# Optimization experiments

Measured on AMD Instinct MI355X. Metric: run time of the kernel, lower is better.

Reference implementation:

```python
import jax, jax.numpy as jnp
import numpy as np

C = 256
CQK = C // 8  # 32


def setup_inputs() -> dict:
    key = jax.random.key(0)
    ks = jax.random.split(key, 7)
    x = jax.random.normal(ks[0], (4, C, 64, 64), dtype=jnp.float32)
    s = 1.0 / np.sqrt(C)
    Wq = jax.random.normal(ks[1], (CQK, C), dtype=jnp.float32) * s
    bq = jnp.zeros((CQK,), dtype=jnp.float32)
    Wk = jax.random.normal(ks[2], (CQK, C), dtype=jnp.float32) * s
    bk = jnp.zeros((CQK,), dtype=jnp.float32)
    Wv = jax.random.normal(ks[3], (C, C), dtype=jnp.float32) * s
    bv = jnp.zeros((C,), dtype=jnp.float32)
    return {"x": x, "Wq": Wq, "bq": bq, "Wk": Wk, "bk": bk, "Wv": Wv, "bv": bv}


def reference(x, Wq, bq, Wk, bk, Wv, bv):
    B, Cc, H, W = x.shape
    xf = x.reshape(B, Cc, H * W)  # [B, C, HW]
    # 1x1 convs == per-pixel linear projections over channels
    q = jnp.einsum('oc,bcn->bno', Wq, xf) + bq          # [B, HW, C//8]
    k = jnp.einsum('oc,bcn->bon', Wk, xf) + bk[:, None]  # [B, C//8, HW]
    v = jnp.einsum('oc,bcn->bno', Wv, xf) + bv          # [B, HW, C]
    attn = jax.nn.softmax(jnp.einsum('bnd,bdm->bnm', q, k), axis=-1)  # [B, HW, HW]
    out = jnp.einsum('bnm,bmc->bnc', attn, v)           # [B, HW, C]
    return out.transpose(0, 2, 1).reshape(B, Cc, H, W)
```

## Files before the change

kernel.cpp:

```cpp
#include <hip/hip_runtime.h>
#include <hip/hip_bf16.h>


#define N_PIX 4096
#define DQK   32
#define CCH   256
#define LOG2E 1.44269504088896f

typedef __attribute__((ext_vector_type(8))) _Float16 f16x8;
typedef __attribute__((ext_vector_type(4))) _Float16 f16x4;
typedef __attribute__((ext_vector_type(2))) _Float16 f16x2;
typedef __attribute__((ext_vector_type(8))) short    bf16x8;
typedef __attribute__((ext_vector_type(4))) short    bf16x4;
typedef __attribute__((ext_vector_type(4))) float    f32x4;

__device__ inline void barrier_lds() {
    asm volatile("" ::: "memory");
    __builtin_amdgcn_s_waitcnt(0xc07f);
    __builtin_amdgcn_s_barrier();
    asm volatile("" ::: "memory");
}

__device__ inline short bf16bits(float f) {
    __hip_bfloat16 h = __float2bfloat16(f);
    return *(short*)&h;
}

__global__ __launch_bounds__(256) void wpack_kernel(
    const float* __restrict__ Wq, const float* __restrict__ Wk,
    const float* __restrict__ Wv, _Float16* __restrict__ Wp)
{
    const int tid   = threadIdx.x;
    const int wflat = blockIdx.x * 4 + (tid >> 6);
    const int lane  = tid & 63;
    const int L15   = lane & 15;
    const int quad  = lane >> 4;
    const int mt    = wflat >> 3;
    const int ks    = wflat & 7;
    const int m0    = mt * 16;

    const float* Wsrc; int row; float scale = 1.f;
    if (m0 < 32)      { Wsrc = Wq; row = m0 + L15;      scale = LOG2E; }
    else if (m0 < 64) { Wsrc = Wk; row = m0 - 32 + L15; }
    else              { Wsrc = Wv; row = m0 - 64 + L15; }

    const float* p = Wsrc + (size_t)row * 256 + ks * 32 + quad * 8;
    f16x8 h;
    #pragma unroll
    for (int j = 0; j < 8; ++j) h[j] = (_Float16)(p[j] * scale);
    *(f16x8*)(Wp + ((size_t)wflat * 64 + lane) * 8) = h;
}

__global__ __launch_bounds__(512, 4) void qkv_kernel(
    const float* __restrict__ x, const _Float16* __restrict__ Wp,
    const float* __restrict__ bq, const float* __restrict__ bk,
    const float* __restrict__ bv,
    _Float16* __restrict__ qo, _Float16* __restrict__ ko,
    __hip_bfloat16* __restrict__ vp)
{
    __shared__ alignas(16) unsigned char shraw[256 * 40 * 2];
    _Float16       (*xT)[264] = (_Float16 (*)[264])shraw;
    __hip_bfloat16 (*vst)[40] = (__hip_bfloat16 (*)[40])shraw;

    const int idx = blockIdx.x;
    const int b   = (idx & 7) >> 1;
    const int n0  = (((idx >> 3) << 1) | (idx & 1)) * 32;
    const int tid = threadIdx.x;

    {
        const float* xb = x + (size_t)b * CCH * N_PIX;
        float4 ld[2][2];
        int c2s[2], n4s[2];
        #pragma unroll
        for (int pass = 0; pass < 2; ++pass) {
            const int flat = pass * 512 + tid;
            c2s[pass] = (flat >> 3) * 2;
            n4s[pass] = (flat & 7) * 4;
            ld[pass][0] = *(const float4*)(xb + (size_t)c2s[pass]       * N_PIX + n0 + n4s[pass]);
            ld[pass][1] = *(const float4*)(xb + (size_t)(c2s[pass] + 1) * N_PIX + n0 + n4s[pass]);
        }
        #pragma unroll
        for (int pass = 0; pass < 2; ++pass) {
            const float a[4] = {ld[pass][0].x, ld[pass][0].y, ld[pass][0].z, ld[pass][0].w};
            const float c[4] = {ld[pass][1].x, ld[pass][1].y, ld[pass][1].z, ld[pass][1].w};
            #pragma unroll
            for (int i = 0; i < 4; ++i)
                *(f16x2*)(&xT[n4s[pass] + i][c2s[pass]]) =
                    (f16x2){(_Float16)a[i], (_Float16)c[i]};
        }
    }
    __syncthreads();

    const int lane = tid & 63;
    const int wid  = tid >> 6;
    const int L15  = lane & 15;
    const int quad = lane >> 4;
    const int nf   = wid & 1;
    const int mtg  = wid >> 1;

    const f32x4 fz = {0.f, 0.f, 0.f, 0.f};
    f32x4 acc[5];
    #pragma unroll
    for (int mt = 0; mt < 5; ++mt) acc[mt] = fz;

    const _Float16* wpw = Wp + ((size_t)(mtg * 5) * 8 * 64 + lane) * 8;

    #pragma unroll
    for (int ks = 0; ks < 8; ++ks) {
        const f16x8 bfr = *(const f16x8*)(&xT[nf * 16 + L15][ks * 32 + quad * 8]);
        #pragma unroll
        for (int mt = 0; mt < 5; ++mt) {
            const f16x8 afr = *(const f16x8*)(wpw + (size_t)(mt * 8 + ks) * 512);
            acc[mt] = __builtin_amdgcn_mfma_f32_16x16x32_f16(afr, bfr, acc[mt], 0, 0, 0);
        }
    }

    const int np = nf * 16 + L15;
    const int n  = n0 + np;
    #pragma unroll
    for (int mt = 0; mt < 5; ++mt) {
        const int m0 = (mtg * 5 + mt) * 16;
        const f32x4 a = acc[mt];
        if (m0 < 32) {
            const int mr = m0 + quad * 4;
            f16x4 h;
            #pragma unroll
            for (int r = 0; r < 4; ++r) h[r] = (_Float16)(a[r] + bq[mr + r] * LOG2E);
            *(f16x4*)(qo + ((size_t)b * N_PIX + n) * DQK + mr) = h;
        } else if (m0 < 64) {
            const int mr = m0 - 32 + quad * 4;
            f16x4 h;
            #pragma unroll
            for (int r = 0; r < 4; ++r) h[r] = (_Float16)(a[r] + bk[mr + r]);
            *(f16x4*)(ko + ((size_t)b * N_PIX + n) * DQK + mr) = h;
        }
    }

    __syncthreads();

    #pragma unroll
    for (int mt = 0; mt < 5; ++mt) {
        const int m0 = (mtg * 5 + mt) * 16;
        if (m0 >= 64) {
            const int c = m0 - 64 + quad * 4;
            #pragma unroll
            for (int r = 0; r < 4; ++r)
                vst[c + r][np] = __float2bfloat16(acc[mt][r] + bv[c + r]);
        }
    }
    __syncthreads();

    {
        __hip_bfloat16* vpb = vp + (size_t)b * 2048 * 512 + (size_t)((n0 >> 5) * 16) * 512;
        #pragma unroll
        for (int s = 0; s < 2; ++s) {
            const int slot = s * 512 + tid;
            const int cg16 = slot >> 6;
            const int ln   = slot & 63;
            const int qd   = ln >> 4;
            const int l15  = ln & 15;
            const bf16x8 val = *(const bf16x8*)(&vst[cg16 * 16 + l15][qd * 8]);
            *(bf16x8*)(vpb + ((size_t)cg16 * 64 + ln) * 8) = val;
        }
    }
}

__global__ __launch_bounds__(1024, 1) void attn_kernel(
    const _Float16* __restrict__ qg,
    const _Float16* __restrict__ kg,
    const __hip_bfloat16* __restrict__ vp,
    float* __restrict__ out)
{
    __shared__ alignas(16) __hip_bfloat16 Ps[2][64][72];
    __shared__ float lsum[4][4][16];

    const int idx  = blockIdx.x;
    const int b    = (idx & 7) >> 1;
    const int n0   = (((idx >> 3) << 1) | (idx & 1)) * 64;
    const int tid  = threadIdx.x;
    const int wid  = tid >> 6;
    const int lane = tid & 63;
    const int L15  = lane & 15;
    const int quad = lane >> 4;
    const int qt   = wid & 3;
    const int kt   = wid >> 2;
    const int qp   = wid & 1;
    const int cg   = wid >> 1;
    const int c0   = cg * 32;

    const f32x4 fz = {0.f, 0.f, 0.f, 0.f};

    const f16x8 aq = *(const f16x8*)(qg + ((size_t)b * N_PIX + n0 + qt * 16 + L15) * DQK + quad * 8);

    f32x4 oacc[2][2];
    #pragma unroll
    for (int qq = 0; qq < 2; ++qq)
        #pragma unroll
        for (int cf = 0; cf < 2; ++cf) oacc[qq][cf] = fz;
    float psum = 0.f;

    const _Float16* kptr =
        kg + (size_t)b * N_PIX * DQK + (size_t)(kt * 16 + L15) * DQK + quad * 8;
    const __hip_bfloat16* vpb = vp + (size_t)b * 2048 * 512 + (size_t)lane * 8;

    const f16x8 k0f = *(const f16x8*)kptr;
    f16x8 kcur = *(const f16x8*)(kptr + 64 * DQK);
    bf16x8 vcur[2][2], vnext[2][2];
    #pragma unroll
    for (int kk = 0; kk < 2; ++kk)
        #pragma unroll
        for (int cf = 0; cf < 2; ++cf) {
            vcur[kk][cf]  = *(const bf16x8*)(vpb + (size_t)((kk)*16     + cg * 2 + cf) * 512);
            vnext[kk][cf] = *(const bf16x8*)(vpb + (size_t)((2 + kk)*16 + cg * 2 + cf) * 512);
        }
    {
        const f32x4 s = __builtin_amdgcn_mfma_f32_16x16x32_f16(k0f, aq, fz, 0, 0, 0);
        bf16x4 pk;
        #pragma unroll
        for (int r = 0; r < 4; ++r) { const float p = exp2f(s[r]); psum += p; pk[r] = bf16bits(p); }
        *(bf16x4*)(&Ps[0][qt * 16 + L15][kt * 16 + quad * 4]) = pk;
    }
    barrier_lds();

    for (int it = 0; it < 64; ++it) {
        const int buf = it & 1;
        const int ld  = (it + 2 < 64) ? it + 2 : 63;

        const f16x8 knew = *(const f16x8*)(kptr + (size_t)ld * 64 * DQK);
        bf16x8 vnew[2][2];
        #pragma unroll
        for (int kk = 0; kk < 2; ++kk)
            #pragma unroll
            for (int cf = 0; cf < 2; ++cf)
                vnew[kk][cf] = *(const bf16x8*)(vpb + (size_t)((ld * 2 + kk) * 16 + cg * 2 + cf) * 512);

        #pragma unroll
        for (int qq = 0; qq < 2; ++qq)
            #pragma unroll
            for (int kk = 0; kk < 2; ++kk) {
                const bf16x8 ap = *(const bf16x8*)(&Ps[buf][(qp * 2 + qq) * 16 + L15][kk * 32 + quad * 8]);
                #pragma unroll
                for (int cf = 0; cf < 2; ++cf)
                    oacc[qq][cf] = __builtin_amdgcn_mfma_f32_16x16x32_bf16(ap, vcur[kk][cf], oacc[qq][cf], 0, 0, 0);
            }

        if (it < 63) {
            const f32x4 s = __builtin_amdgcn_mfma_f32_16x16x32_f16(kcur, aq, fz, 0, 0, 0);
            bf16x4 pk;
            #pragma unroll
            for (int r = 0; r < 4; ++r) { const float p = exp2f(s[r]); psum += p; pk[r] = bf16bits(p); }
            *(bf16x4*)(&Ps[buf ^ 1][qt * 16 + L15][kt * 16 + quad * 4]) = pk;
        }
        barrier_lds();

        kcur = knew;
        #pragma unroll
        for (int kk = 0; kk < 2; ++kk)
            #pragma unroll
            for (int cf = 0; cf < 2; ++cf) {
                vcur[kk][cf]  = vnext[kk][cf];
                vnext[kk][cf] = vnew[kk][cf];
            }
    }

    psum += __shfl_xor(psum, 16, 64);
    psum += __shfl_xor(psum, 32, 64);
    if (quad == 0) lsum[qt][kt][L15] = psum;
    __syncthreads();

    float* ob = out + (size_t)b * CCH * N_PIX;
    #pragma unroll
    for (int qq = 0; qq < 2; ++qq) {
        const int qtile = qp * 2 + qq;
        float inv_l[4];
        #pragma unroll
        for (int r = 0; r < 4; ++r) {
            const int q = quad * 4 + r;
            inv_l[r] = 1.f / (lsum[qtile][0][q] + lsum[qtile][1][q] +
                              lsum[qtile][2][q] + lsum[qtile][3][q]);
        }
        #pragma unroll
        for (int cf = 0; cf < 2; ++cf) {
            const int c = c0 + cf * 16 + L15;
            f32x4 o;
            #pragma unroll
            for (int r = 0; r < 4; ++r) o[r] = oacc[qq][cf][r] * inv_l[r];
            *(f32x4*)(ob + (size_t)c * N_PIX + n0 + qtile * 16 + quad * 4) = o;
        }
    }
}

extern "C" void kernel_launch(void* const* d_in, const int* in_sizes, int n_in,
                              void* d_out, int out_size, void* d_ws, size_t ws_size,
                              hipStream_t stream) {
    (void)in_sizes; (void)n_in; (void)out_size; (void)ws_size;
    const float* x  = (const float*)d_in[0];
    const float* Wq = (const float*)d_in[1];
    const float* bq = (const float*)d_in[2];
    const float* Wk = (const float*)d_in[3];
    const float* bk = (const float*)d_in[4];
    const float* Wv = (const float*)d_in[5];
    const float* bv = (const float*)d_in[6];

    _Float16* qb = (_Float16*)d_ws;
    _Float16* kb = qb + (size_t)4 * N_PIX * DQK;
    __hip_bfloat16* vpk = (__hip_bfloat16*)(kb + (size_t)4 * N_PIX * DQK);
    _Float16* wp = (_Float16*)(vpk + (size_t)4 * 2048 * 512);
    float* outp = (float*)d_out;

    wpack_kernel<<<40, 256, 0, stream>>>(Wq, Wk, Wv, wp);
    qkv_kernel<<<512, 512, 0, stream>>>(x, wp, bq, bk, bv, qb, kb, vpk);
    attn_kernel<<<256, 1024, 0, stream>>>(qb, kb, vpk, outp);
}
```

Baseline: 147.4 us.

## Fuse weight pack, QKV projection and attention into one cooperative kernel

Merges the three launches (weight packing, QKV projection, attention) into a single cooperative kernel of 256 blocks of 1024 threads, separated by grid-wide syncs. Each block now projects 64 pixels instead of 32 and reuses one shared-memory buffer for all phases. The goal is to remove launch gaps and inter-kernel drain and fill. In exchange it adds two grid barriers, and the QKV phase gets fewer, larger blocks with lower occupancy. It also adds an unroll-2 pragma on the attention loop.

```diff
diff --git a/kernel.cpp b/kernel.cpp
--- a/kernel.cpp
+++ b/kernel.cpp
@@ -1,5 +1,8 @@
 #include <hip/hip_runtime.h>
 #include <hip/hip_bf16.h>
+#include <hip/hip_cooperative_groups.h>
+
+namespace cg = cooperative_groups;
 
 
 #define N_PIX 4096
@@ -26,266 +29,251 @@
     return *(short*)&h;
 }
 
-__global__ __launch_bounds__(256) void wpack_kernel(
-    const float* __restrict__ Wq, const float* __restrict__ Wk,
-    const float* __restrict__ Wv, _Float16* __restrict__ Wp)
-{
-    const int tid   = threadIdx.x;
-    const int wflat = blockIdx.x * 4 + (tid >> 6);
-    const int lane  = tid & 63;
-    const int L15   = lane & 15;
-    const int quad  = lane >> 4;
-    const int mt    = wflat >> 3;
-    const int ks    = wflat & 7;
-    const int m0    = mt * 16;
-
-    const float* Wsrc; int row; float scale = 1.f;
-    if (m0 < 32)      { Wsrc = Wq; row = m0 + L15;      scale = LOG2E; }
-    else if (m0 < 64) { Wsrc = Wk; row = m0 - 32 + L15; }
-    else              { Wsrc = Wv; row = m0 - 64 + L15; }
-
-    const float* p = Wsrc + (size_t)row * 256 + ks * 32 + quad * 8;
-    f16x8 h;
-    #pragma unroll
-    for (int j = 0; j < 8; ++j) h[j] = (_Float16)(p[j] * scale);
-    *(f16x8*)(Wp + ((size_t)wflat * 64 + lane) * 8) = h;
-}
-
-__global__ __launch_bounds__(512, 4) void qkv_kernel(
-    const float* __restrict__ x, const _Float16* __restrict__ Wp,
-    const float* __restrict__ bq, const float* __restrict__ bk,
-    const float* __restrict__ bv,
+__global__ __launch_bounds__(1024, 1) void fused_kernel(
+    const float* __restrict__ x,
+    const float* __restrict__ Wq, const float* __restrict__ bq,
+    const float* __restrict__ Wk, const float* __restrict__ bk,
+    const float* __restrict__ Wv, const float* __restrict__ bv,
     _Float16* __restrict__ qo, _Float16* __restrict__ ko,
-    __hip_bfloat16* __restrict__ vp)
-{
-    __shared__ alignas(16) unsigned char shraw[256 * 40 * 2];
-    _Float16       (*xT)[264] = (_Float16 (*)[264])shraw;
-    __hip_bfloat16 (*vst)[40] = (__hip_bfloat16 (*)[40])shraw;
-
-    const int idx = blockIdx.x;
-    const int b   = (idx & 7) >> 1;
-    const int n0  = (((idx >> 3) << 1) | (idx & 1)) * 32;
-    const int tid = threadIdx.x;
-
-    {
-        const float* xb = x + (size_t)b * CCH * N_PIX;
-        float4 ld[2][2];
-        int c2s[2], n4s[2];
-        #pragma unroll
-        for (int pass = 0; pass < 2; ++pass) {
-            const int flat = pass * 512 + tid;
-            c2s[pass] = (flat >> 3) * 2;
-            n4s[pass] = (flat & 7) * 4;
-            ld[pass][0] = *(const float4*)(xb + (size_t)c2s[pass]       * N_PIX + n0 + n4s[pass]);
-            ld[pass][1] = *(const float4*)(xb + (size_t)(c2s[pass] + 1) * N_PIX + n0 + n4s[pass]);
-        }
-        #pragma unroll
-        for (int pass = 0; pass < 2; ++pass) {
-            const float a[4] = {ld[pass][0].x, ld[pass][0].y, ld[pass][0].z, ld[pass][0].w};
-            const float c[4] = {ld[pass][1].x, ld[pass][1].y, ld[pass][1].z, ld[pass][1].w};
-            #pragma unroll
-            for (int i = 0; i < 4; ++i)
-                *(f16x2*)(&xT[n4s[pass] + i][c2s[pass]]) =
-                    (f16x2){(_Float16)a[i], (_Float16)c[i]};
-        }
-    }
-    __syncthreads();
-
-    const int lane = tid & 63;
-    const int wid  = tid >> 6;
-    const int L15  = lane & 15;
-    const int quad = lane >> 4;
-    const int nf   = wid & 1;
-    const int mtg  = wid >> 1;
-
-    const f32x4 fz = {0.f, 0.f, 0.f, 0.f};
-    f32x4 acc[5];
-    #pragma unroll
-    for (int mt = 0; mt < 5; ++mt) acc[mt] = fz;
-
-    const _Float16* wpw = Wp + ((size_t)(mtg * 5) * 8 * 64 + lane) * 8;
-
-    #pragma unroll
-    for (int ks = 0; ks < 8; ++ks) {
-        const f16x8 bfr = *(const f16x8*)(&xT[nf * 16 + L15][ks * 32 + quad * 8]);
-        #pragma unroll
-        for (int mt = 0; mt < 5; ++mt) {
-            const f16x8 afr = *(const f16x8*)(wpw + (size_t)(mt * 8 + ks) * 512);
-            acc[mt] = __builtin_amdgcn_mfma_f32_16x16x32_f16(afr, bfr, acc[mt], 0, 0, 0);
-        }
-    }
-
-    const int np = nf * 16 + L15;
-    const int n  = n0 + np;
-    #pragma unroll
-    for (int mt = 0; mt < 5; ++mt) {
-        const int m0 = (mtg * 5 + mt) * 16;
-        const f32x4 a = acc[mt];
-        if (m0 < 32) {
-            const int mr = m0 + quad * 4;
-            f16x4 h;
-            #pragma unroll
-            for (int r = 0; r < 4; ++r) h[r] = (_Float16)(a[r] + bq[mr + r] * LOG2E);
-            *(f16x4*)(qo + ((size_t)b * N_PIX + n) * DQK + mr) = h;
-        } else if (m0 < 64) {
-            const int mr = m0 - 32 + quad * 4;
-            f16x4 h;
-            #pragma unroll
-            for (int r = 0; r < 4; ++r) h[r] = (_Float16)(a[r] + bk[mr + r]);
-            *(f16x4*)(ko + ((size_t)b * N_PIX + n) * DQK + mr) = h;
-        }
-    }
-
-    __syncthreads();
-
-    #pragma unroll
-    for (int mt = 0; mt < 5; ++mt) {
-        const int m0 = (mtg * 5 + mt) * 16;
-        if (m0 >= 64) {
-            const int c = m0 - 64 + quad * 4;
-            #pragma unroll
-            for (int r = 0; r < 4; ++r)
-                vst[c + r][np] = __float2bfloat16(acc[mt][r] + bv[c + r]);
-        }
-    }
-    __syncthreads();
-
-    {
-        __hip_bfloat16* vpb = vp + (size_t)b * 2048 * 512 + (size_t)((n0 >> 5) * 16) * 512;
-        #pragma unroll
-        for (int s = 0; s < 2; ++s) {
-            const int slot = s * 512 + tid;
-            const int cg16 = slot >> 6;
-            const int ln   = slot & 63;
-            const int qd   = ln >> 4;
-            const int l15  = ln & 15;
-            const bf16x8 val = *(const bf16x8*)(&vst[cg16 * 16 + l15][qd * 8]);
-            *(bf16x8*)(vpb + ((size_t)cg16 * 64 + ln) * 8) = val;
-        }
-    }
-}
-
-__global__ __launch_bounds__(1024, 1) void attn_kernel(
-    const _Float16* __restrict__ qg,
-    const _Float16* __restrict__ kg,
-    const __hip_bfloat16* __restrict__ vp,
+    __hip_bfloat16* __restrict__ vp,
+    _Float16* __restrict__ Wp,
     float* __restrict__ out)
 {
-    __shared__ alignas(16) __hip_bfloat16 Ps[2][64][72];
-    __shared__ float lsum[4][4][16];
+    __shared__ alignas(16) unsigned char shraw[36864];
+    _Float16       (*xT)[264]     = (_Float16 (*)[264])shraw;
+    __hip_bfloat16 (*vst)[72]     = (__hip_bfloat16 (*)[72])shraw;
+    __hip_bfloat16 (*Ps)[64][72]  = (__hip_bfloat16 (*)[64][72])shraw;
+    float          (*lsum)[4][16] = (float (*)[4][16])(shraw + 2 * 64 * 72 * 2);
 
     const int idx  = blockIdx.x;
-    const int b    = (idx & 7) >> 1;
-    const int n0   = (((idx >> 3) << 1) | (idx & 1)) * 64;
     const int tid  = threadIdx.x;
     const int wid  = tid >> 6;
     const int lane = tid & 63;
     const int L15  = lane & 15;
     const int quad = lane >> 4;
-    const int qt   = wid & 3;
-    const int kt   = wid >> 2;
-    const int qp   = wid & 1;
-    const int cg   = wid >> 1;
-    const int c0   = cg * 32;
+
+    const int b  = (idx & 7) >> 1;
+    const int nt = ((idx >> 3) << 1) | (idx & 1);
+    const int n0 = nt * 64;
 
     const f32x4 fz = {0.f, 0.f, 0.f, 0.f};
 
-    const f16x8 aq = *(const f16x8*)(qg + ((size_t)b * N_PIX + n0 + qt * 16 + L15) * DQK + quad * 8);
-
-    f32x4 oacc[2][2];
-    #pragma unroll
-    for (int qq = 0; qq < 2; ++qq)
-        #pragma unroll
-        for (int cf = 0; cf < 2; ++cf) oacc[qq][cf] = fz;
-    float psum = 0.f;
-
-    const _Float16* kptr =
-        kg + (size_t)b * N_PIX * DQK + (size_t)(kt * 16 + L15) * DQK + quad * 8;
-    const __hip_bfloat16* vpb = vp + (size_t)b * 2048 * 512 + (size_t)lane * 8;
-
-    const f16x8 k0f = *(const f16x8*)kptr;
-    f16x8 kcur = *(const f16x8*)(kptr + 64 * DQK);
-    bf16x8 vcur[2][2], vnext[2][2];
-    #pragma unroll
-    for (int kk = 0; kk < 2; ++kk)
-        #pragma unroll
-        for (int cf = 0; cf < 2; ++cf) {
-            vcur[kk][cf]  = *(const bf16x8*)(vpb + (size_t)((kk)*16     + cg * 2 + cf) * 512);
-            vnext[kk][cf] = *(const bf16x8*)(vpb + (size_t)((2 + kk)*16 + cg * 2 + cf) * 512);
-        }
     {
-        const f32x4 s = __builtin_amdgcn_mfma_f32_16x16x32_f16(k0f, aq, fz, 0, 0, 0);
-        bf16x4 pk;
-        #pragma unroll
-        for (int r = 0; r < 4; ++r) { const float p = exp2f(s[r]); psum += p; pk[r] = bf16bits(p); }
-        *(bf16x4*)(&Ps[0][qt * 16 + L15][kt * 16 + quad * 4]) = pk;
+        const float* xb = x + (size_t)b * CCH * N_PIX;
+        float4 ld[2][2];
+        int c2s[2], n4s[2];
+        #pragma unroll
+        for (int pass = 0; pass < 2; ++pass) {
+            const int flat = pass * 1024 + tid;
+            c2s[pass] = (flat >> 4) * 2;
+            n4s[pass] = (flat & 15) * 4;
+            ld[pass][0] = *(const float4*)(xb + (size_t)c2s[pass]       * N_PIX + n0 + n4s[pass]);
+            ld[pass][1] = *(const float4*)(xb + (size_t)(c2s[pass] + 1) * N_PIX + n0 + n4s[pass]);
+        }
+        #pragma unroll
+        for (int pass = 0; pass < 2; ++pass) {
+            const float a[4] = {ld[pass][0].x, ld[pass][0].y, ld[pass][0].z, ld[pass][0].w};
+            const float c[4] = {ld[pass][1].x, ld[pass][1].y, ld[pass][1].z, ld[pass][1].w};
+            #pragma unroll
+            for (int i = 0; i < 4; ++i)
+                *(f16x2*)(&xT[n4s[pass] + i][c2s[pass]]) =
+                    (f16x2){(_Float16)a[i], (_Float16)c[i]};
+        }
     }
-    barrier_lds();
-
-    for (int it = 0; it < 64; ++it) {
-        const int buf = it & 1;
-        const int ld  = (it + 2 < 64) ? it + 2 : 63;
-
-        const f16x8 knew = *(const f16x8*)(kptr + (size_t)ld * 64 * DQK);
-        bf16x8 vnew[2][2];
+
+    if (idx < 10) {
+        const int wflat = idx * 16 + wid;
+        const int mt    = wflat >> 3;
+        const int ks    = wflat & 7;
+        const int m0    = mt * 16;
+        const float* Wsrc; int row; float scale = 1.f;
+        if (m0 < 32)      { Wsrc = Wq; row = m0 + L15;      scale = LOG2E; }
+        else if (m0 < 64) { Wsrc = Wk; row = m0 - 32 + L15; }
+        else              { Wsrc = Wv; row = m0 - 64 + L15; }
+        const float* p = Wsrc + (size_t)row * 256 + ks * 32 + quad * 8;
+        f16x8 h;
+        #pragma unroll
+        for (int j = 0; j < 8; ++j) h[j] = (_Float16)(p[j] * scale);
+        *(f16x8*)(Wp + ((size_t)wflat * 64 + lane) * 8) = h;
+    }
+
+    cg::this_grid().sync();
+
+    {
+        const int nf  = wid & 3;
+        const int mtg = wid >> 2;
+
+        f32x4 acc[5];
+        #pragma unroll
+        for (int mt = 0; mt < 5; ++mt) acc[mt] = fz;
+
+        const _Float16* wpw = Wp + ((size_t)(mtg * 5) * 8 * 64 + lane) * 8;
+
+        #pragma unroll
+        for (int ks = 0; ks < 8; ++ks) {
+            const f16x8 bfr = *(const f16x8*)(&xT[nf * 16 + L15][ks * 32 + quad * 8]);
+            #pragma unroll
+            for (int mt = 0; mt < 5; ++mt) {
+                const f16x8 afr = *(const f16x8*)(wpw + (size_t)(mt * 8 + ks) * 512);
+                acc[mt] = __builtin_amdgcn_mfma_f32_16x16x32_f16(afr, bfr, acc[mt], 0, 0, 0);
+            }
+        }
+
+        const int np = nf * 16 + L15;
+        const int n  = n0 + np;
+        #pragma unroll
+        for (int mt = 0; mt < 5; ++mt) {
+            const int m0 = (mtg * 5 + mt) * 16;
+            const f32x4 a = acc[mt];
+            if (m0 < 32) {
+                const int mr = m0 + quad * 4;
+                f16x4 h;
+                #pragma unroll
+                for (int r = 0; r < 4; ++r) h[r] = (_Float16)(a[r] + bq[mr + r] * LOG2E);
+                *(f16x4*)(qo + ((size_t)b * N_PIX + n) * DQK + mr) = h;
+            } else if (m0 < 64) {
+                const int mr = m0 - 32 + quad * 4;
+                f16x4 h;
+                #pragma unroll
+                for (int r = 0; r < 4; ++r) h[r] = (_Float16)(a[r] + bk[mr + r]);
+                *(f16x4*)(ko + ((size_t)b * N_PIX + n) * DQK + mr) = h;
+            }
+        }
+
+        __syncthreads();
+
+        #pragma unroll
+        for (int mt = 0; mt < 5; ++mt) {
+            const int m0 = (mtg * 5 + mt) * 16;
+            if (m0 >= 64) {
+                const int c = m0 - 64 + quad * 4;
+                #pragma unroll
+                for (int r = 0; r < 4; ++r)
+                    vst[c + r][np] = __float2bfloat16(acc[mt][r] + bv[c + r]);
+            }
+        }
+        __syncthreads();
+
+        __hip_bfloat16* vpb0 = vp + (size_t)b * 2048 * 512 + (size_t)(nt * 2) * 16 * 512;
+        #pragma unroll
+        for (int s = 0; s < 2; ++s) {
+            const int slot = s * 1024 + tid;
+            const int nch  = slot >> 10;
+            const int rem  = slot & 1023;
+            const int cg16 = rem >> 6;
+            const int ln   = rem & 63;
+            const bf16x8 val = *(const bf16x8*)(&vst[cg16 * 16 + (ln & 15)][nch * 32 + (ln >> 4) * 8]);
+            *(bf16x8*)(vpb0 + ((size_t)(nch * 16 + cg16) * 64 + ln) * 8) = val;
+        }
+    }
+
+    cg::this_grid().sync();
+
+    {
+        const int qt = wid & 3;
+        const int kt = wid >> 2;
+        const int qp = wid & 1;
+        const int cg = wid >> 1;
+        const int c0 = cg * 32;
+
+        const f16x8 aq = *(const f16x8*)(qo + ((size_t)b * N_PIX + n0 + qt * 16 + L15) * DQK + quad * 8);
+
+        f32x4 oacc[2][2];
+        #pragma unroll
+        for (int qq = 0; qq < 2; ++qq)
+            #pragma unroll
+            for (int cf = 0; cf < 2; ++cf) oacc[qq][cf] = fz;
+        float psum = 0.f;
+
+        const _Float16* kptr =
+            ko + (size_t)b * N_PIX * DQK + (size_t)(kt * 16 + L15) * DQK + quad * 8;
+        const __hip_bfloat16* vpb = vp + (size_t)b * 2048 * 512 + (size_t)lane * 8;
+
+        const f16x8 k0f = *(const f16x8*)kptr;
+        f16x8 kcur = *(const f16x8*)(kptr + 64 * DQK);
+        bf16x8 vcur[2][2], vnext[2][2];
         #pragma unroll
         for (int kk = 0; kk < 2; ++kk)
             #pragma unroll
-            for (int cf = 0; cf < 2; ++cf)
-                vnew[kk][cf] = *(const bf16x8*)(vpb + (size_t)((ld * 2 + kk) * 16 + cg * 2 + cf) * 512);
-
-        #pragma unroll
-        for (int qq = 0; qq < 2; ++qq)
-            #pragma unroll
-            for (int kk = 0; kk < 2; ++kk) {
-                const bf16x8 ap = *(const bf16x8*)(&Ps[buf][(qp * 2 + qq) * 16 + L15][kk * 32 + quad * 8]);
+            for (int cf = 0; cf < 2; ++cf) {
+                vcur[kk][cf]  = *(const bf16x8*)(vpb + (size_t)(kk * 16       + cg * 2 + cf) * 512);
+                vnext[kk][cf] = *(const bf16x8*)(vpb + (size_t)((2 + kk) * 16 + cg * 2 + cf) * 512);
+            }
+        {
+            const f32x4 s = __builtin_amdgcn_mfma_f32_16x16x32_f16(k0f, aq, fz, 0, 0, 0);
+            bf16x4 pk;
+            #pragma unroll
+            for (int r = 0; r < 4; ++r) { const float p = exp2f(s[r]); psum += p; pk[r] = bf16bits(p); }
+            *(bf16x4*)(&Ps[0][qt * 16 + L15][kt * 16 + quad * 4]) = pk;
+        }
+        barrier_lds();
+
+        #pragma unroll 2
+        for (int it = 0; it < 64; ++it) {
+            const int buf = it & 1;
+            const int ld  = (it + 2 < 64) ? it + 2 : 63;
+
+            const f16x8 knew = *(const f16x8*)(kptr + (size_t)ld * 64 * DQK);
+            bf16x8 vnew[2][2];
+            #pragma unroll
+            for (int kk = 0; kk < 2; ++kk)
                 #pragma unroll
                 for (int cf = 0; cf < 2; ++cf)
-                    oacc[qq][cf] = __builtin_amdgcn_mfma_f32_16x16x32_bf16(ap, vcur[kk][cf], oacc[qq][cf], 0, 0, 0);
-            }
-
-        if (it < 63) {
-            const f32x4 s = __builtin_amdgcn_mfma_f32_16x16x32_f16(kcur, aq, fz, 0, 0, 0);
-            bf16x4 pk;
-            #pragma unroll
-            for (int r = 0; r < 4; ++r) { const float p = exp2f(s[r]); psum += p; pk[r] = bf16bits(p); }
-            *(bf16x4*)(&Ps[buf ^ 1][qt * 16 + L15][kt * 16 + quad * 4]) = pk;
-        }
-        barrier_lds();
-
-        kcur = knew;
-        #pragma unroll
-        for (int kk = 0; kk < 2; ++kk)
+                    vnew[kk][cf] = *(const bf16x8*)(vpb + (size_t)((ld * 2 + kk) * 16 + cg * 2 + cf) * 512);
+
+            #pragma unroll
+            for (int qq = 0; qq < 2; ++qq)
+                #pragma unroll
+                for (int kk = 0; kk < 2; ++kk) {
+                    const bf16x8 ap = *(const bf16x8*)(&Ps[buf][(qp * 2 + qq) * 16 + L15][kk * 32 + quad * 8]);
+                    #pragma unroll
+                    for (int cf = 0; cf < 2; ++cf)
+                        oacc[qq][cf] = __builtin_amdgcn_mfma_f32_16x16x32_bf16(ap, vcur[kk][cf], oacc[qq][cf], 0, 0, 0);
+                }
+
+            if (it < 63) {
+                const f32x4 s = __builtin_amdgcn_mfma_f32_16x16x32_f16(kcur, aq, fz, 0, 0, 0);
+                bf16x4 pk;
+                #pragma unroll
+                for (int r = 0; r < 4; ++r) { const float p = exp2f(s[r]); psum += p; pk[r] = bf16bits(p); }
+                *(bf16x4*)(&Ps[buf ^ 1][qt * 16 + L15][kt * 16 + quad * 4]) = pk;
+            }
+            barrier_lds();
+
+            kcur = knew;
+            #pragma unroll
+            for (int kk = 0; kk < 2; ++kk)
+                #pragma unroll
+                for (int cf = 0; cf < 2; ++cf) {
+                    vcur[kk][cf]  = vnext[kk][cf];
+                    vnext[kk][cf] = vnew[kk][cf];
+                }
+        }
+
+        psum += __shfl_xor(psum, 16, 64);
+        psum += __shfl_xor(psum, 32, 64);
+        if (quad == 0) lsum[qt][kt][L15] = psum;
+        __syncthreads();
+
+        float* ob = out + (size_t)b * CCH * N_PIX;
+        #pragma unroll
+        for (int qq = 0; qq < 2; ++qq) {
+            const int qtile = qp * 2 + qq;
+            float inv_l[4];
+            #pragma unroll
+            for (int r = 0; r < 4; ++r) {
+                const int q = quad * 4 + r;
+                inv_l[r] = 1.f / (lsum[qtile][0][q] + lsum[qtile][1][q] +
+                                  lsum[qtile][2][q] + lsum[qtile][3][q]);
+            }
             #pragma unroll
             for (int cf = 0; cf < 2; ++cf) {
-                vcur[kk][cf]  = vnext[kk][cf];
-                vnext[kk][cf] = vnew[kk][cf];
-            }
-    }
-
-    psum += __shfl_xor(psum, 16, 64);
-    psum += __shfl_xor(psum, 32, 64);
-    if (quad == 0) lsum[qt][kt][L15] = psum;
-    __syncthreads();
-
-    float* ob = out + (size_t)b * CCH * N_PIX;
-    #pragma unroll
-    for (int qq = 0; qq < 2; ++qq) {
-        const int qtile = qp * 2 + qq;
-        float inv_l[4];
-        #pragma unroll
-        for (int r = 0; r < 4; ++r) {
-            const int q = quad * 4 + r;
-            inv_l[r] = 1.f / (lsum[qtile][0][q] + lsum[qtile][1][q] +
-                              lsum[qtile][2][q] + lsum[qtile][3][q]);
-        }
-        #pragma unroll
-        for (int cf = 0; cf < 2; ++cf) {
-            const int c = c0 + cf * 16 + L15;
-            f32x4 o;
-            #pragma unroll
-            for (int r = 0; r < 4; ++r) o[r] = oacc[qq][cf][r] * inv_l[r];
-            *(f32x4*)(ob + (size_t)c * N_PIX + n0 + qtile * 16 + quad * 4) = o;
+                const int c = c0 + cf * 16 + L15;
+                f32x4 o;
+                #pragma unroll
+                for (int r = 0; r < 4; ++r) o[r] = oacc[qq][cf][r] * inv_l[r];
+                *(f32x4*)(ob + (size_t)c * N_PIX + n0 + qtile * 16 + quad * 4) = o;
+            }
         }
     }
 }
@@ -308,7 +296,9 @@
     _Float16* wp = (_Float16*)(vpk + (size_t)4 * 2048 * 512);
     float* outp = (float*)d_out;
 
-    wpack_kernel<<<40, 256, 0, stream>>>(Wq, Wk, Wv, wp);
-    qkv_kernel<<<512, 512, 0, stream>>>(x, wp, bq, bk, bv, qb, kb, vpk);
-    attn_kernel<<<256, 1024, 0, stream>>>(qb, kb, vpk, outp);
+    void* args[] = { (void*)&x, (void*)&Wq, (void*)&bq, (void*)&Wk, (void*)&bk,
+                     (void*)&Wv, (void*)&bv, (void*)&qb, (void*)&kb, (void*)&vpk,
+                     (void*)&wp, (void*)&outp };
+    hipLaunchCooperativeKernel((const void*)fused_kernel, dim3(256), dim3(1024),
+                               args, 0, stream);
 }
```

Measured after the change: 220.0 us. 49.2% more time.

## Double key-tile width per iteration to halve barriers in attention loop

Applied to the files above, without the earlier changes.

The attention main loop now processes 128 keys per iteration instead of 64. The P tile in LDS is widened to match, and each wave computes two score MFMAs per step. K and V prefetch uses double-buffered register arrays indexed by iteration parity, with the loop unrolled by two. The aim is to halve the number of block-wide barriers and amortize loop overhead over more MFMA work, at the cost of more registers and LDS.

```diff
diff --git a/kernel.cpp b/kernel.cpp
--- a/kernel.cpp
+++ b/kernel.cpp
@@ -157,9 +157,7 @@
             const int slot = s * 512 + tid;
             const int cg16 = slot >> 6;
             const int ln   = slot & 63;
-            const int qd   = ln >> 4;
-            const int l15  = ln & 15;
-            const bf16x8 val = *(const bf16x8*)(&vst[cg16 * 16 + l15][qd * 8]);
+            const bf16x8 val = *(const bf16x8*)(&vst[cg16 * 16 + (ln & 15)][(ln >> 4) * 8]);
             *(bf16x8*)(vpb + ((size_t)cg16 * 64 + ln) * 8) = val;
         }
     }
@@ -171,7 +169,7 @@
     const __hip_bfloat16* __restrict__ vp,
     float* __restrict__ out)
 {
-    __shared__ alignas(16) __hip_bfloat16 Ps[2][64][72];
+    __shared__ alignas(16) __hip_bfloat16 Ps[2][64][136];
     __shared__ float lsum[4][4][16];
 
     const int idx  = blockIdx.x;
@@ -199,68 +197,75 @@
         for (int cf = 0; cf < 2; ++cf) oacc[qq][cf] = fz;
     float psum = 0.f;
 
-    const _Float16* kptr =
+    const _Float16* kbase =
         kg + (size_t)b * N_PIX * DQK + (size_t)(kt * 16 + L15) * DQK + quad * 8;
     const __hip_bfloat16* vpb = vp + (size_t)b * 2048 * 512 + (size_t)lane * 8;
 
-    const f16x8 k0f = *(const f16x8*)kptr;
-    f16x8 kcur = *(const f16x8*)(kptr + 64 * DQK);
-    bf16x8 vcur[2][2], vnext[2][2];
-    #pragma unroll
-    for (int kk = 0; kk < 2; ++kk)
-        #pragma unroll
-        for (int cf = 0; cf < 2; ++cf) {
-            vcur[kk][cf]  = *(const bf16x8*)(vpb + (size_t)((kk)*16     + cg * 2 + cf) * 512);
-            vnext[kk][cf] = *(const bf16x8*)(vpb + (size_t)((2 + kk)*16 + cg * 2 + cf) * 512);
-        }
+    f16x8 kc[2][2];
+    bf16x8 vb[2][4][2];
     {
-        const f32x4 s = __builtin_amdgcn_mfma_f32_16x16x32_f16(k0f, aq, fz, 0, 0, 0);
-        bf16x4 pk;
-        #pragma unroll
-        for (int r = 0; r < 4; ++r) { const float p = exp2f(s[r]); psum += p; pk[r] = bf16bits(p); }
-        *(bf16x4*)(&Ps[0][qt * 16 + L15][kt * 16 + quad * 4]) = pk;
-    }
-    barrier_lds();
-
-    for (int it = 0; it < 64; ++it) {
-        const int buf = it & 1;
-        const int ld  = (it + 2 < 64) ? it + 2 : 63;
-
-        const f16x8 knew = *(const f16x8*)(kptr + (size_t)ld * 64 * DQK);
-        bf16x8 vnew[2][2];
-        #pragma unroll
-        for (int kk = 0; kk < 2; ++kk)
-            #pragma unroll
-            for (int cf = 0; cf < 2; ++cf)
-                vnew[kk][cf] = *(const bf16x8*)(vpb + (size_t)((ld * 2 + kk) * 16 + cg * 2 + cf) * 512);
-
-        #pragma unroll
-        for (int qq = 0; qq < 2; ++qq)
-            #pragma unroll
-            for (int kk = 0; kk < 2; ++kk) {
-                const bf16x8 ap = *(const bf16x8*)(&Ps[buf][(qp * 2 + qq) * 16 + L15][kk * 32 + quad * 8]);
+        #pragma unroll
+        for (int h = 0; h < 2; ++h) {
+            const f16x8 k0 = *(const f16x8*)(kbase + (size_t)(h * 64) * DQK);
+            const f32x4 s  = __builtin_amdgcn_mfma_f32_16x16x32_f16(k0, aq, fz, 0, 0, 0);
+            bf16x4 pk;
+            #pragma unroll
+            for (int r = 0; r < 4; ++r) { const float p = exp2f(s[r]); psum += p; pk[r] = bf16bits(p); }
+            *(bf16x4*)(&Ps[0][qt * 16 + L15][(kt + 4 * h) * 16 + quad * 4]) = pk;
+        }
+        #pragma unroll
+        for (int h = 0; h < 2; ++h) {
+            kc[1][h] = *(const f16x8*)(kbase + (size_t)(128 + h * 64) * DQK);
+            kc[0][h] = *(const f16x8*)(kbase + (size_t)(256 + h * 64) * DQK);
+        }
+        #pragma unroll
+        for (int p2 = 0; p2 < 2; ++p2)
+            #pragma unroll
+            for (int kk = 0; kk < 4; ++kk)
                 #pragma unroll
                 for (int cf = 0; cf < 2; ++cf)
-                    oacc[qq][cf] = __builtin_amdgcn_mfma_f32_16x16x32_bf16(ap, vcur[kk][cf], oacc[qq][cf], 0, 0, 0);
+                    vb[p2][kk][cf] = *(const bf16x8*)(vpb + (size_t)((p2 * 4 + kk) * 16 + cg * 2 + cf) * 512);
+    }
+    barrier_lds();
+
+    #pragma unroll 2
+    for (int SI = 0; SI < 32; ++SI) {
+        const int p = SI & 1;
+
+        #pragma unroll
+        for (int kk = 0; kk < 4; ++kk)
+            #pragma unroll
+            for (int qq = 0; qq < 2; ++qq) {
+                const bf16x8 ap = *(const bf16x8*)(&Ps[p][(qp * 2 + qq) * 16 + L15][kk * 32 + quad * 8]);
+                #pragma unroll
+                for (int cf = 0; cf < 2; ++cf)
+                    oacc[qq][cf] = __builtin_amdgcn_mfma_f32_16x16x32_bf16(ap, vb[p][kk][cf], oacc[qq][cf], 0, 0, 0);
             }
 
-        if (it < 63) {
-            const f32x4 s = __builtin_amdgcn_mfma_f32_16x16x32_f16(kcur, aq, fz, 0, 0, 0);
-            bf16x4 pk;
-            #pragma unroll
-            for (int r = 0; r < 4; ++r) { const float p = exp2f(s[r]); psum += p; pk[r] = bf16bits(p); }
-            *(bf16x4*)(&Ps[buf ^ 1][qt * 16 + L15][kt * 16 + quad * 4]) = pk;
+        if (SI < 31) {
+            #pragma unroll
+            for (int h = 0; h < 2; ++h) {
+                const f32x4 s = __builtin_amdgcn_mfma_f32_16x16x32_f16(kc[p ^ 1][h], aq, fz, 0, 0, 0);
+                bf16x4 pk;
+                #pragma unroll
+                for (int r = 0; r < 4; ++r) { const float pv = exp2f(s[r]); psum += pv; pk[r] = bf16bits(pv); }
+                *(bf16x4*)(&Ps[p ^ 1][qt * 16 + L15][(kt + 4 * h) * 16 + quad * 4]) = pk;
+            }
+        }
+
+        {
+            const int ksi = (SI + 3 < 32) ? SI + 3 : 31;
+            #pragma unroll
+            for (int h = 0; h < 2; ++h)
+                kc[p ^ 1][h] = *(const f16x8*)(kbase + ((size_t)ksi * 128 + h * 64) * DQK);
+            const int vsi = (SI + 2 < 32) ? SI + 2 : 31;
+            #pragma unroll
+            for (int kk = 0; kk < 4; ++kk)
+                #pragma unroll
+                for (int cf = 0; cf < 2; ++cf)
+                    vb[p][kk][cf] = *(const bf16x8*)(vpb + (size_t)((vsi * 4 + kk) * 16 + cg * 2 + cf) * 512);
         }
         barrier_lds();
-
-        kcur = knew;
-        #pragma unroll
-        for (int kk = 0; kk < 2; ++kk)
-            #pragma unroll
-            for (int cf = 0; cf < 2; ++cf) {
-                vcur[kk][cf]  = vnext[kk][cf];
-                vnext[kk][cf] = vnew[kk][cf];
-            }
     }
 
     psum += __shfl_xor(psum, 16, 64);
```

Measured after the change: 153.4 us. 1.04x slower.
